# Kernel tuning notes

Measured on AMD Instinct MI355X. Metric: run time of the kernel, lower is better.

The kernel has to match this reference:

```python
import jax, jax.numpy as jnp
import numpy as np

GMIN = 0.01
GMAX = 10.0


def _ptanh(x, eta):
    # printed tanh-style learnable activation: eta0 + eta1 * tanh((x - eta2) * eta3)
    return eta[0] + eta[1] * jnp.tanh((x - eta[2]) * eta[3])


def setup_inputs() -> dict:
    key = jax.random.key(0)
    k1, k2 = jax.random.split(key)
    B, n_in, n_out = 32768, 256, 256
    a_previous = jax.random.uniform(k1, (B, n_in), dtype=jnp.float32)
    eta_act = jnp.array([0.0, 1.0, 0.5, 2.0], dtype=jnp.float32)
    eta_inv = jnp.array([1.0, -1.0, 0.5, 2.0], dtype=jnp.float32)
    # theta init exactly as in pLayer.__init__
    theta = jax.random.uniform(k2, (n_in + 2, n_out), dtype=jnp.float32) / 100.0 + GMIN
    theta = theta.at[-1, :].add(GMAX)
    ratio = eta_act[2] / (1.0 - eta_act[2])  # eta2/(1-eta2)
    theta = theta.at[-2, :].set(ratio * (jnp.sum(theta[:-2, :], axis=0) + theta[-1, :]))
    return {"a_previous": a_previous, "theta_": theta, "eta_act": eta_act, "eta_inv": eta_inv}


def reference(a_previous, theta_, eta_act, eta_inv):
    # clamp + threshold-to-zero (forward value of the straight-through theta)
    theta = jnp.clip(theta_, -GMAX, GMAX)
    theta = jnp.where(jnp.abs(theta) < GMIN, 0.0, theta)
    # normalized conductance weights
    abs_t = jnp.abs(theta)
    W = abs_t / jnp.sum(abs_t, axis=0, keepdims=True)  # [n_in+2, n_out]
    pos = (theta >= 0.0).astype(theta.dtype)
    neg = 1.0 - pos
    B = a_previous.shape[0]
    ones = jnp.ones((B, 1), dtype=a_previous.dtype)
    zeros = jnp.zeros((B, 1), dtype=a_previous.dtype)
    a_ext = jnp.concatenate([a_previous, ones, zeros], axis=1)  # [B, n_in+2]
    a_neg = _ptanh(a_ext, eta_inv).at[:, -1].set(0.0)  # inverter, last (dummy) col zeroed
    z = a_ext @ (W * pos) + a_neg @ (W * neg)  # [B, n_out]
    return _ptanh(z, eta_act)
```

## Files before the change

### kernel.cpp

```cpp
#include <hip/hip_runtime.h>
#include <hip/hip_bf16.h>

typedef unsigned int u32;
typedef __attribute__((ext_vector_type(8))) _Float16 f16x8;
typedef __attribute__((ext_vector_type(4))) float f32x4;

#define GMIN_ 0.01f
#define GMAX_ 10.0f

__device__ __forceinline__ float tanh_fast2(float y2) {
    float e = __expf(y2);
    float r = __builtin_amdgcn_rcpf(e + 1.0f);
    return fmaf(-2.0f, r, 1.0f);
}

__global__ __launch_bounds__(256) void prep_weights(
    const float* __restrict__ theta, const float* __restrict__ eta_inv,
    _Float16* __restrict__ W2t, float* __restrict__ bias)
{
    __shared__ float tile[258][17];
    __shared__ float psum[16][17];
    __shared__ float cinv[16];

    const int t  = threadIdx.x;
    const int kq = t >> 4;
    const int nl = t & 15;
    const int n  = blockIdx.x * 16 + nl;

    float part = 0.f;
#pragma unroll
    for (int i = 0; i < 17; ++i) {
        const int k = i * 16 + kq;
        if (k < 258) {
            float tt = theta[k * 256 + n];
            tt = fminf(fmaxf(tt, -GMAX_), GMAX_);
            if (fabsf(tt) < GMIN_) tt = 0.f;
            tile[k][nl] = tt;
            part += fabsf(tt);
        }
    }
    psum[kq][nl] = part;
    __syncthreads();
    if (kq == 0) {
        float s = 0.f;
#pragma unroll
        for (int j = 0; j < 16; ++j) s += psum[j][nl];
        cinv[nl] = 1.0f / s;
    }
    __syncthreads();

    const int nw = t >> 4;
    const int kc = t & 15;
    const float inv = cinv[nw];
    const int nn = blockIdx.x * 16 + nw;
#pragma unroll
    for (int c = 0; c < 4; ++c) {
        f16x8 h;
#pragma unroll
        for (int e = 0; e < 4; ++e) {
            const float tt = tile[kc * 16 + c * 4 + e][nw];
            const float w  = fabsf(tt) * inv;
            const float wp = (tt >= 0.f) ? w : 0.f;
            h[2 * e]     = (_Float16)wp;
            h[2 * e + 1] = (_Float16)(w - wp);
        }
        *(f16x8*)(W2t + (size_t)nn * 512 + kc * 32 + c * 8) = h;
    }

    if (t < 16) {
        const float tt = tile[256][t];
        const float w  = fabsf(tt) * cinv[t];
        const float wp = (tt >= 0.f) ? w : 0.f;
        const float wn = w - wp;
        const float ei0 = eta_inv[0], ei1 = eta_inv[1], ei2 = eta_inv[2], ei3 = eta_inv[3];
        const float a1  = ei0 + ei1 * tanhf((1.0f - ei2) * ei3);
        bias[blockIdx.x * 16 + t] = wp + a1 * wn;
    }
}

__global__ __launch_bounds__(256, 4) void plax_gemm(
    const float* __restrict__ A, const _Float16* __restrict__ W2t,
    const float* __restrict__ bias, const float* __restrict__ eta_act,
    const float* __restrict__ eta_inv, float* __restrict__ out)
{
    __shared__ __align__(16) char Bs[2][16384];

    const int t    = threadIdx.x;
    const int bid  = blockIdx.x;
    const int swz  = ((bid & 7) << 7) | (bid >> 3);
    const int mblk = swz >> 2;
    const int nblk = swz & 3;
    const int lane = t & 63, wave = t >> 6;
    const int lr   = lane & 15, lg = lane >> 4;

    const float ei0 = eta_inv[0], ei1 = eta_inv[1];
    const float k2i = 2.0f * eta_inv[3];
    const float c2i = 2.0f * eta_inv[2] * eta_inv[3];

    const int row0 = mblk * 128 + wave * 32;
    const int col0 = nblk * 64;

    const float* ap = A + (size_t)(row0 + lr) * 256 + lg * 4;

    const _Float16* bsrc[4];
    char*           bdst[4];
#pragma unroll
    for (int q = 0; q < 4; ++q) {
        const int idx  = q * 256 + t;
        const int col  = idx >> 4;
        const int slot = idx & 15;
        bsrc[q] = W2t + (size_t)(col0 + col) * 512 + slot * 8;
        bdst[q] = (char*)&Bs[0][0] + col * 256 + ((slot ^ (col & 15)) * 16);
    }

    f32x4 acc[2][4] = {};

#define LDA(it, dst) do {                                         \
        dst[0] = *(const float4*)(ap + (it) * 16);                \
        dst[1] = *(const float4*)(ap + 4096 + (it) * 16);         \
    } while (0)

    float4 aqA[2], aqB[2];
    LDA(0, aqA);

    f16x8 breg[4];
#pragma unroll
    for (int q = 0; q < 4; ++q) breg[q] = *(const f16x8*)(bsrc[q]);
#pragma unroll
    for (int q = 0; q < 4; ++q) *(f16x8*)(bdst[q]) = breg[q];
    asm volatile("s_waitcnt lgkmcnt(0)" ::: "memory");
    __builtin_amdgcn_sched_barrier(0);
    __builtin_amdgcn_s_barrier();

#pragma unroll
    for (int r = 0; r < 4; ++r) {
        if (r < 3) {
#pragma unroll
            for (int q = 0; q < 4; ++q)
                breg[q] = *(const f16x8*)(bsrc[q] + (r + 1) * 128);
        }

        const char* buf = (const char*)&Bs[r & 1][0];
#pragma unroll
        for (int j = 0; j < 4; ++j) {
            const int it = r * 4 + j;
            if (it + 1 < 16) {
                if (it & 1) LDA(it + 1, aqA); else LDA(it + 1, aqB);
            }
            const float4* acur = (it & 1) ? aqB : aqA;

            f16x8 af[2];
#pragma unroll
            for (int m = 0; m < 2; ++m) {
                const float4 v = acur[m];
                f16x8 h;
                h[0] = (_Float16)v.x;
                h[1] = (_Float16)fmaf(ei1, tanh_fast2(fmaf(v.x, k2i, -c2i)), ei0);
                h[2] = (_Float16)v.y;
                h[3] = (_Float16)fmaf(ei1, tanh_fast2(fmaf(v.y, k2i, -c2i)), ei0);
                h[4] = (_Float16)v.z;
                h[5] = (_Float16)fmaf(ei1, tanh_fast2(fmaf(v.z, k2i, -c2i)), ei0);
                h[6] = (_Float16)v.w;
                h[7] = (_Float16)fmaf(ei1, tanh_fast2(fmaf(v.w, k2i, -c2i)), ei0);
                af[m] = h;
            }

            f16x8 bf[4];
#pragma unroll
            for (int n = 0; n < 4; ++n) {
                const int rr   = n * 16 + lr;
                const int phys = (j * 4 + lg) ^ (rr & 15);
                bf[n] = *(const f16x8*)(buf + rr * 256 + phys * 16);
            }

#pragma unroll
            for (int m = 0; m < 2; ++m)
#pragma unroll
                for (int n = 0; n < 4; ++n)
                    acc[m][n] = __builtin_amdgcn_mfma_f32_16x16x32_f16(
                        af[m], bf[n], acc[m][n], 0, 0, 0);
        }

        if (r < 3) {
            __builtin_amdgcn_s_barrier();
            const int off = ((r + 1) & 1) * 16384;
#pragma unroll
            for (int q = 0; q < 4; ++q)
                *(f16x8*)(bdst[q] + off) = breg[q];
            asm volatile("s_waitcnt lgkmcnt(0)" ::: "memory");
            __builtin_amdgcn_sched_barrier(0);
            __builtin_amdgcn_s_barrier();
        }
    }
#undef LDA

    const float ea0 = eta_act[0], ea1 = eta_act[1];
    const float k2a = 2.0f * eta_act[3];
    const float c2a = 2.0f * eta_act[2] * eta_act[3];

    float bc[4];
#pragma unroll
    for (int n = 0; n < 4; ++n) bc[n] = bias[col0 + n * 16 + lr];

#pragma unroll
    for (int m = 0; m < 2; ++m) {
        const int rgb = row0 + m * 16 + lg * 4;
#pragma unroll
        for (int n = 0; n < 4; ++n) {
            const int cg = col0 + n * 16 + lr;
#pragma unroll
            for (int j = 0; j < 4; ++j) {
                const float z = acc[m][n][j] + bc[n];
                out[(size_t)(rgb + j) * 256 + cg] =
                    fmaf(ea1, tanh_fast2(fmaf(z, k2a, -c2a)), ea0);
            }
        }
    }
}

extern "C" void kernel_launch(void* const* d_in, const int* in_sizes, int n_in,
                              void* d_out, int out_size, void* d_ws, size_t ws_size,
                              hipStream_t stream) {
    (void)in_sizes; (void)n_in; (void)out_size; (void)ws_size;
    const float* a       = (const float*)d_in[0];
    const float* theta   = (const float*)d_in[1];
    const float* eta_act = (const float*)d_in[2];
    const float* eta_inv = (const float*)d_in[3];
    float* out = (float*)d_out;

    _Float16* W2t  = (_Float16*)d_ws;
    float*    bias = (float*)((char*)d_ws + 256 * 512 * 2);

    prep_weights<<<16, 256, 0, stream>>>(theta, eta_inv, W2t, bias);
    plax_gemm<<<1024, 256, 0, stream>>>(a, W2t, bias, eta_act, eta_inv, out);
}
```

Baseline: 110.5 us.

## Stage weights via direct global-to-LDS loads, deepen A prefetch, use exp2 tanh

Replaces the register round-trip for weight tiles (global load into VGPRs, then an LDS store) with global_load_lds, which writes straight into a double-buffered LDS tile. The XOR swizzle moves into the global source address. The activation loads are now prefetched three iterations ahead through a four-slot register ring instead of double buffering. The tanh helpers fold log2(e) into their constants so they can call the exp2 builtin directly. The aim is to cut VGPR pressure and LDS-store instructions and to hide global-load latency better. The cost is more live registers for the A ring and reliance on vmcnt waits for LDS visibility.

```diff
diff --git a/kernel.cpp b/kernel.cpp
--- a/kernel.cpp
+++ b/kernel.cpp
@@ -7,9 +7,10 @@
 
 #define GMIN_ 0.01f
 #define GMAX_ 10.0f
-
-__device__ __forceinline__ float tanh_fast2(float y2) {
-    float e = __expf(y2);
+#define LOG2E_ 1.4426950408889634f
+
+__device__ __forceinline__ float tanh_exp2(float y2l) {
+    float e = __builtin_amdgcn_exp2f(y2l);
     float r = __builtin_amdgcn_rcpf(e + 1.0f);
     return fmaf(-2.0f, r, 1.0f);
 }
@@ -94,74 +95,67 @@
     const int lr   = lane & 15, lg = lane >> 4;
 
     const float ei0 = eta_inv[0], ei1 = eta_inv[1];
-    const float k2i = 2.0f * eta_inv[3];
-    const float c2i = 2.0f * eta_inv[2] * eta_inv[3];
+    const float k2i = 2.0f * eta_inv[3] * LOG2E_;
+    const float c2i = 2.0f * eta_inv[2] * eta_inv[3] * LOG2E_;
 
     const int row0 = mblk * 128 + wave * 32;
     const int col0 = nblk * 64;
 
     const float* ap = A + (size_t)(row0 + lr) * 256 + lg * 4;
 
-    const _Float16* bsrc[4];
-    char*           bdst[4];
-#pragma unroll
-    for (int q = 0; q < 4; ++q) {
-        const int idx  = q * 256 + t;
-        const int col  = idx >> 4;
-        const int slot = idx & 15;
-        bsrc[q] = W2t + (size_t)(col0 + col) * 512 + slot * 8;
-        bdst[q] = (char*)&Bs[0][0] + col * 256 + ((slot ^ (col & 15)) * 16);
-    }
+    const char* bsrc = (const char*)W2t
+        + (size_t)(col0 + (t >> 4)) * 1024
+        + (size_t)(((t & 15) ^ (t >> 4)) * 16);
 
     f32x4 acc[2][4] = {};
-
-#define LDA(it, dst) do {                                         \
-        dst[0] = *(const float4*)(ap + (it) * 16);                \
-        dst[1] = *(const float4*)(ap + 4096 + (it) * 16);         \
+    float4 aq[4][2];
+
+#define LDA(it_) do {                                               \
+        aq[(it_) & 3][0] = *(const float4*)(ap + (it_) * 16);       \
+        aq[(it_) & 3][1] = *(const float4*)(ap + 4096 + (it_) * 16);\
     } while (0)
 
-    float4 aqA[2], aqB[2];
-    LDA(0, aqA);
-
-    f16x8 breg[4];
-#pragma unroll
-    for (int q = 0; q < 4; ++q) breg[q] = *(const f16x8*)(bsrc[q]);
-#pragma unroll
-    for (int q = 0; q < 4; ++q) *(f16x8*)(bdst[q]) = breg[q];
-    asm volatile("s_waitcnt lgkmcnt(0)" ::: "memory");
+#define STAGE_B(r_, bb_) do {                                                   \
+        _Pragma("unroll")                                                       \
+        for (int i_ = 0; i_ < 4; ++i_)                                          \
+            __builtin_amdgcn_global_load_lds(                                   \
+                (const __attribute__((address_space(1))) u32*)                  \
+                    (bsrc + (size_t)i_ * 16384 + (size_t)(r_) * 256),           \
+                (__attribute__((address_space(3))) u32*)                        \
+                    ((char*)Bs + (bb_) * 16384 + i_ * 4096 + t * 16),           \
+                16, 0, 0);                                                      \
+    } while (0)
+
+    STAGE_B(0, 0);
+    asm volatile("s_waitcnt vmcnt(0)" ::: "memory");
     __builtin_amdgcn_sched_barrier(0);
     __builtin_amdgcn_s_barrier();
+    LDA(0); LDA(1); LDA(2);
 
 #pragma unroll
     for (int r = 0; r < 4; ++r) {
-        if (r < 3) {
-#pragma unroll
-            for (int q = 0; q < 4; ++q)
-                breg[q] = *(const f16x8*)(bsrc[q] + (r + 1) * 128);
-        }
-
-        const char* buf = (const char*)&Bs[r & 1][0];
+        if (r < 3) STAGE_B(r + 1, (r + 1) & 1);
+
+        const char* buf = (const char*)Bs + (r & 1) * 16384;
 #pragma unroll
         for (int j = 0; j < 4; ++j) {
             const int it = r * 4 + j;
-            if (it + 1 < 16) {
-                if (it & 1) LDA(it + 1, aqA); else LDA(it + 1, aqB);
-            }
-            const float4* acur = (it & 1) ? aqB : aqA;
-
+            if (it + 3 < 16) LDA(it + 3);
+
+            const float4* acur = aq[it & 3];
             f16x8 af[2];
 #pragma unroll
             for (int m = 0; m < 2; ++m) {
                 const float4 v = acur[m];
                 f16x8 h;
                 h[0] = (_Float16)v.x;
-                h[1] = (_Float16)fmaf(ei1, tanh_fast2(fmaf(v.x, k2i, -c2i)), ei0);
+                h[1] = (_Float16)fmaf(ei1, tanh_exp2(fmaf(v.x, k2i, -c2i)), ei0);
                 h[2] = (_Float16)v.y;
-                h[3] = (_Float16)fmaf(ei1, tanh_fast2(fmaf(v.y, k2i, -c2i)), ei0);
+                h[3] = (_Float16)fmaf(ei1, tanh_exp2(fmaf(v.y, k2i, -c2i)), ei0);
                 h[4] = (_Float16)v.z;
-                h[5] = (_Float16)fmaf(ei1, tanh_fast2(fmaf(v.z, k2i, -c2i)), ei0);
+                h[5] = (_Float16)fmaf(ei1, tanh_exp2(fmaf(v.z, k2i, -c2i)), ei0);
                 h[6] = (_Float16)v.w;
-                h[7] = (_Float16)fmaf(ei1, tanh_fast2(fmaf(v.w, k2i, -c2i)), ei0);
+                h[7] = (_Float16)fmaf(ei1, tanh_exp2(fmaf(v.w, k2i, -c2i)), ei0);
                 af[m] = h;
             }
 
@@ -169,7 +163,7 @@
 #pragma unroll
             for (int n = 0; n < 4; ++n) {
                 const int rr   = n * 16 + lr;
-                const int phys = (j * 4 + lg) ^ (rr & 15);
+                const int phys = (j * 4 + lg) ^ lr;
                 bf[n] = *(const f16x8*)(buf + rr * 256 + phys * 16);
             }
 
@@ -182,21 +176,17 @@
         }
 
         if (r < 3) {
-            __builtin_amdgcn_s_barrier();
-            const int off = ((r + 1) & 1) * 16384;
-#pragma unroll
-            for (int q = 0; q < 4; ++q)
-                *(f16x8*)(bdst[q] + off) = breg[q];
-            asm volatile("s_waitcnt lgkmcnt(0)" ::: "memory");
+            asm volatile("s_waitcnt vmcnt(0)" ::: "memory");
             __builtin_amdgcn_sched_barrier(0);
             __builtin_amdgcn_s_barrier();
         }
     }
 #undef LDA
+#undef STAGE_B
 
     const float ea0 = eta_act[0], ea1 = eta_act[1];
-    const float k2a = 2.0f * eta_act[3];
-    const float c2a = 2.0f * eta_act[2] * eta_act[3];
+    const float k2a = 2.0f * eta_act[3] * LOG2E_;
+    const float c2a = 2.0f * eta_act[2] * eta_act[3] * LOG2E_;
 
     float bc[4];
 #pragma unroll
@@ -212,7 +202,7 @@
             for (int j = 0; j < 4; ++j) {
                 const float z = acc[m][n][j] + bc[n];
                 out[(size_t)(rgb + j) * 256 + cg] =
-                    fmaf(ea1, tanh_fast2(fmaf(z, k2a, -c2a)), ea0);
+                    fmaf(ea1, tanh_exp2(fmaf(z, k2a, -c2a)), ea0);
             }
         }
     }
```

Measured after the change: 107.1 us. -3.1%, faster.
